# Kernel tuning notes

Hardware: AMD Instinct MI355X
Metric: run time of the kernel (lower is better)

The kernel has to match this reference:

```python
import jax, jax.numpy as jnp
import numpy as np
from jax import lax

B, NF, NOBJ, SZ = 16, 4, 32, 128
HALF = SZ // 2  # 64


def _build_grid(h, w):
    ys = jnp.linspace(0.0, 1.0, h)
    xs = jnp.linspace(0.0, 1.0, w)
    gy, gx = jnp.meshgrid(ys, xs, indexing='ij')
    g = jnp.stack([gy, gx], axis=-1)  # (H, W, 2)
    return jnp.concatenate([g, 1.0 - g], axis=-1)[None]  # (1, H, W, 4)


def setup_inputs() -> dict:
    key = jax.random.key(0)
    ks = jax.random.split(key, 8)
    images = jax.random.normal(ks[0], (B, 3 * NF, SZ, SZ), dtype=jnp.float32)
    rois = jax.random.randint(ks[1], (B, NOBJ, SZ, SZ), 0, 2).astype(jnp.bool_)
    conv1_w = jax.random.normal(ks[2], (64, 3 * NF, 3, 3), dtype=jnp.float32) * 0.05
    conv1_b = jnp.zeros((64,), dtype=jnp.float32)
    conv2_w = jax.random.normal(ks[3], (128, 64, 3, 3), dtype=jnp.float32) * 0.05
    conv2_b = jnp.zeros((128,), dtype=jnp.float32)
    dense_w = jax.random.normal(ks[4], (128, 4), dtype=jnp.float32) * 0.1
    dense_b = jnp.zeros((128,), dtype=jnp.float32)
    return dict(images=images, rois=rois, conv1_w=conv1_w, conv1_b=conv1_b,
                conv2_w=conv2_w, conv2_b=conv2_b, dense_w=dense_w, dense_b=dense_b)


def _conv(x, w, b):
    y = lax.conv_general_dilated(x, w, window_strides=(1, 1), padding='SAME',
                                 dimension_numbers=('NCHW', 'OIHW', 'NCHW'))
    return y + b[None, :, None, None]


def reference(images, rois, conv1_w, conv1_b, conv2_w, conv2_b, dense_w, dense_b):
    # conv stack
    x = jax.nn.relu(_conv(images, conv1_w, conv1_b))
    x = lax.reduce_window(x, -jnp.inf, lax.max, (1, 1, 2, 2), (1, 1, 2, 2), 'VALID')
    x = jax.nn.relu(_conv(x, conv2_w, conv2_b))  # (B, 128, 64, 64)
    # soft position embed
    grid = _build_grid(HALF, HALF)  # (1, 64, 64, 4)
    pe = grid @ dense_w.T + dense_b  # (1, 64, 64, 128)
    x = x + jnp.transpose(pe, (0, 3, 1, 2))  # (B, 128, 64, 64)
    # roi pool: nearest-downsample masks 128->64 (indices 0,2,4,...)
    r = rois[:, :, ::2, ::2].astype(x.dtype)  # (B, O, 64, 64)
    masked = x[:, None] * r[:, :, None]  # (B, O, 128, 64, 64)
    return jnp.max(masked, axis=(-2, -1))  # (B, O, 128)
```

## Files before the change

### kernel.cpp

```cpp
#include <hip/hip_runtime.h>


typedef __attribute__((ext_vector_type(8))) short short8;
typedef __attribute__((ext_vector_type(4))) float f32x4;
typedef __attribute__((ext_vector_type(4))) unsigned short us4;
typedef __attribute__((ext_vector_type(2))) unsigned short u16x2;
typedef unsigned short u16;
typedef unsigned int u32;

__device__ __forceinline__ u16 f2bf(float f) {
  u32 u = __builtin_bit_cast(u32, f);
  return (u16)((u + 0x7fffu + ((u >> 16) & 1u)) >> 16);
}

__device__ __forceinline__ u32 pkmaxu(u32 a, u32 b) {
  u16x2 x = __builtin_bit_cast(u16x2, a), y = __builtin_bit_cast(u16x2, b);
  return __builtin_bit_cast(u32, __builtin_elementwise_max(x, y));
}
__device__ __forceinline__ u32 map2(u32 v) {
  u32 flip = ((v & 0x80008000u) >> 15) * 0xFFFFu;
  return v ^ (flip | 0x80008000u);
}
__device__ __forceinline__ float unmap1(u32 m) {
  u32 b = m ^ ((m & 0x8000u) ? 0x8000u : 0xFFFFu);
  return __builtin_bit_cast(float, b << 16);
}
__device__ __forceinline__ float fand(float x, u32 m) {
  return __builtin_bit_cast(float, __builtin_bit_cast(u32, x) & m);
}

namespace {

__global__ __launch_bounds__(256) void kio(const float* __restrict__ img,
                                           u16* __restrict__ imgT,
                                           const unsigned* __restrict__ rois,
                                           unsigned* __restrict__ rmask) {
  __shared__ alignas(16) u16 ST[2048];
  const int bx = blockIdx.x;
  const int t = threadIdx.x;
  if (bx < 2048) {
    const int row = bx & 127, b = bx >> 7;
#pragma unroll
    for (int i = 0; i < 2; ++i) {
      const int e = i * 256 + t;
      ST[(e >> 2) * 16 + 12 + (e & 3)] = 0;
    }
#pragma unroll
    for (int i = 0; i < 6; ++i) {
      const int e = i * 256 + t;
      const int ci = e >> 7, col = e & 127;
      const float v = img[(((size_t)(b * 12 + ci)) << 14) + row * 128 + col];
      ST[col * 16 + ci] = f2bf(v);
    }
    __syncthreads();
    us4* dst = (us4*)(imgT + (((size_t)(b * 128 + row)) << 11));
#pragma unroll
    for (int i = 0; i < 2; ++i) {
      const int q = i * 256 + t;
      dst[q] = *(const us4*)&ST[q * 4];
    }
  } else {
    const int lane = t & 63;
    u32 ok = 1u;
#pragma unroll
    for (int i = 0; i < 4; ++i) {
      u32 v = rois[lane * 4 + i];
      ok &= ((v <= 1u) || (v == 0x3f800000u)) ? 1u : 0u;
    }
    const bool isWord = (__all((int)ok) != 0);
    const unsigned char* roisB = (const unsigned char*)rois;
    const int pi = (bx - 2048) * 256 + t;
    const int b = pi >> 11;
    const int pp = pi & 2047;
    const int h = pp >> 5;
    const int wp = pp & 31;
    const size_t base = (size_t)b * 32 * 16384 + (size_t)(2 * h) * 128 + 4 * wp;
    u32 m0 = 0, m1 = 0;
#pragma unroll
    for (int o = 0; o < 32; ++o) {
      const size_t idx = base + (size_t)o * 16384;
      if (isWord) {
        const uint4 q = *(const uint4*)&rois[idx];
        m0 |= (u32)(q.x != 0u) << o;
        m1 |= (u32)(q.z != 0u) << o;
      } else {
        const u32 q = *(const u32*)&roisB[idx];
        m0 |= (u32)((q & 0xffu) != 0u) << o;
        m1 |= (u32)((q & 0xff0000u) != 0u) << o;
      }
    }
    *(uint2*)&rmask[b * 4096 + h * 64 + wp * 2] = make_uint2(m0, m1);
  }
}

__global__ __launch_bounds__(256) void kprep(const float* __restrict__ w2,
                                             u16* __restrict__ Aw,
                                             const float* __restrict__ w1,
                                             u16* __restrict__ Aw1) {
  const int bx = blockIdx.x;
  if (bx < 288) {
    const int idx = bx * 256 + threadIdx.x;
    const int j = idx & 7;
    const int lane = (idx >> 3) & 63;
    const int t3 = idx >> 9;
    const int ks = t3 % 18, cot = t3 / 18;
    const int m = lane & 15, g = lane >> 4;
    const int co = cot * 16 + m;
    const int k = ks * 32 + g * 8 + j;
    const int rc = k >> 6, ci = k & 63;
    Aw[idx] = f2bf(w2[co * 576 + ci * 9 + rc]);
  } else {
    const int idx = (bx - 288) * 256 + threadIdx.x;
    const int j = idx & 7;
    const int lane = (idx >> 3) & 63;
    const int t3 = idx >> 9;
    const int ks = t3 % 5, cot = t3 / 5;
    const int m = lane & 15, g = lane >> 4;
    const int co = cot * 16 + m;
    const int k = ks * 32 + g * 8 + j;
    const int rc = k >> 4, cip = k & 15;
    const float v = (rc < 9 && cip < 12) ? w1[co * 108 + cip * 9 + rc] : 0.f;
    Aw1[idx] = f2bf(v);
  }
}

__global__ __launch_bounds__(256) void k1_mfma(const u16* __restrict__ imgT,
                                               const u16* __restrict__ Aw1,
                                               const float* __restrict__ b1,
                                               u16* __restrict__ pooledT) {
  __shared__ alignas(16) u16 SIMG[8192];
  __shared__ alignas(16) u16 PT[64 * 68];
  const int h2 = blockIdx.x, b = blockIdx.y;
  const int t = threadIdx.x, wv = t >> 6, l = t & 63;

#pragma unroll
  for (int i = 0; i < 4; ++i) {
    const int q = i * 256 + t;
    const int sr = q >> 8, off = q & 255;
    const int irow = 2 * h2 - 1 + sr;
    short8 v = {0, 0, 0, 0, 0, 0, 0, 0};
    if ((unsigned)irow < 128u)
      v = *(const short8*)(imgT + (((size_t)(b * 128 + irow)) << 11) + off * 8);
    *(short8*)((char*)SIMG + ((q * 16) ^ (((q >> 3) & 1) << 4))) = v;
  }
  __syncthreads();

  const int m16 = l & 15, g = l >> 4;
  const int colhalf = wv >> 1, cotbase = (wv & 1) * 2;
  const int cipb = (g & 1) * 16;
  f32x4 acc[2][8];
#pragma unroll
  for (int ct = 0; ct < 2; ++ct)
#pragma unroll
    for (int pt = 0; pt < 8; ++pt) acc[ct][pt] = (f32x4){0.f, 0.f, 0.f, 0.f};

  const u16* awb = Aw1 + (size_t)l * 8;
  const short8 z8 = {0, 0, 0, 0, 0, 0, 0, 0};

#pragma unroll
  for (int ks = 0; ks < 5; ++ks) {
    short8 a0 = *(const short8*)(awb + (cotbase * 5 + ks) * 512);
    short8 a1 = *(const short8*)(awb + ((cotbase + 1) * 5 + ks) * 512);
    const bool pz = (ks == 4) && (g >= 2);
    const int rc = pz ? 0 : (2 * ks + (g >> 1));
    const int rr = (rc * 11) >> 5;
    const int cc = rc - rr * 3;
    const int d = m16 - 1 + cc;
    const int sb = (d < 0) ? 1 : ((d >> 2) & 1);
    const int base = rr * 4096 + d * 32 + colhalf * 2048 + (cipb ^ (sb << 4));
    const bool killLo = (cc == 0) && (m16 == 0) && (colhalf == 0);
    const bool killHi = (cc == 2) && (m16 == 15) && (colhalf == 1);
#pragma unroll
    for (int pt = 0; pt < 8; ++pt) {
      const int r01 = pt >> 2, ct2 = pt & 3;
      short8 bv = *(const short8*)((const char*)SIMG + base + r01 * 4096 + ct2 * 512);
      bool kill = pz;
      if (ct2 == 0) kill = kill || killLo;
      if (ct2 == 3) kill = kill || killHi;
      if (kill) bv = z8;
      acc[0][pt] = __builtin_amdgcn_mfma_f32_16x16x32_bf16(a0, bv, acc[0][pt], 0, 0, 0);
      acc[1][pt] = __builtin_amdgcn_mfma_f32_16x16x32_bf16(a1, bv, acc[1][pt], 0, 0, 0);
    }
  }

#pragma unroll
  for (int ct = 0; ct < 2; ++ct) {
    const int cot = cotbase + ct;
#pragma unroll
    for (int r = 0; r < 4; ++r) {
      const int co = cot * 16 + g * 4 + r;
      const float bias = b1[co];
#pragma unroll
      for (int ct2 = 0; ct2 < 4; ++ct2) {
        float v0 = fmaxf(acc[ct][ct2][r] + bias, 0.f);
        float v1 = fmaxf(acc[ct][4 + ct2][r] + bias, 0.f);
        float vv = fmaxf(v0, v1);
        vv = fmaxf(vv, __shfl_xor(vv, 1, 64));
        if (!(m16 & 1)) {
          const int pw = colhalf * 32 + ct2 * 8 + (m16 >> 1);
          PT[pw * 68 + co] = f2bf(vv);
        }
      }
    }
  }
  __syncthreads();
  u16* dst = pooledT + (((size_t)(b * 64 + h2)) << 12);
#pragma unroll
  for (int i = 0; i < 4; ++i) {
    const int e = (i * 256 + t) * 4;
    const int pw = e >> 6, co = e & 63;
    *(us4*)(dst + e) = *(const us4*)&PT[pw * 68 + co];
  }
}

__global__ __launch_bounds__(256) void k2_mfma(const u16* __restrict__ pooledT,
                                               const u16* __restrict__ Aw,
                                               const float* __restrict__ b2,
                                               const float* __restrict__ dw,
                                               const float* __restrict__ db,
                                               u16* __restrict__ x2b) {
  __shared__ alignas(16) short8 SIN8[1536];
  char* SB = (char*)SIN8;
  const int h = blockIdx.x, b = blockIdx.y;
  const int t = threadIdx.x, wv = t >> 6, l = t & 63;

#pragma unroll
  for (int i = 0; i < 6; ++i) {
    const int chunk = i * 4 + wv;
    const int row = chunk >> 3;
    const int hin = h - 1 + row;
    short8 v = {0, 0, 0, 0, 0, 0, 0, 0};
    if ((unsigned)hin < 64u)
      v = *(const short8*)(pooledT + (((size_t)(b * 64 + hin)) << 12) +
                           ((chunk & 7) << 9) + l * 8);
    const int lin = chunk * 1024 + l * 16;
    *(short8*)(SB + (lin ^ (((lin >> 7) & 7) << 4))) = v;
  }
  __syncthreads();

  const int m16 = l & 15, g = l >> 4;
  const int kbyte = g * 16;
  f32x4 acc[2][4];
#pragma unroll
  for (int ct = 0; ct < 2; ++ct)
#pragma unroll
    for (int n = 0; n < 4; ++n) acc[ct][n] = (f32x4){0.f, 0.f, 0.f, 0.f};

  const u16* aw0 = Aw + (size_t)wv * 36 * 512 + l * 8;
  const short8 z8 = {0, 0, 0, 0, 0, 0, 0, 0};

#pragma unroll
  for (int ks = 0; ks < 18; ++ks) {
    const int rc = ks >> 1, r = rc / 3, c = rc % 3;
    const int koff = r * 8192 + (ks & 1) * 64 + kbyte;
    short8 a0 = *(const short8*)(aw0 + ks * 512);
    short8 a1 = *(const short8*)(aw0 + (18 + ks) * 512);
    const int d = m16 + c - 1;
    const int base = (koff + d * 128) ^ ((d & 7) << 4);
    const bool edgeLo = (c == 0) && (m16 == 0);
    const bool edgeHi = (c == 2) && (m16 == 15);
#pragma unroll
    for (int n = 0; n < 4; ++n) {
      short8 bv = *(const short8*)(SB + base + n * 2048);
      if (c == 0 && n == 0) { if (edgeLo) bv = z8; }
      if (c == 2 && n == 3) { if (edgeHi) bv = z8; }
      acc[0][n] = __builtin_amdgcn_mfma_f32_16x16x32_bf16(a0, bv, acc[0][n], 0, 0, 0);
      acc[1][n] = __builtin_amdgcn_mfma_f32_16x16x32_bf16(a1, bv, acc[1][n], 0, 0, 0);
    }
  }

  const float inv63 = 1.f / 63.f;
  const float gy = (float)h * inv63;
#pragma unroll
  for (int ct = 0; ct < 2; ++ct) {
    const int cot = wv * 2 + ct;
#pragma unroll
    for (int r = 0; r < 4; ++r) {
      const int co = cot * 16 + g * 4 + r;
      const float bias = b2[co];
      const float W0 = dw[co * 4 + 0], W1 = dw[co * 4 + 1];
      const float W2 = dw[co * 4 + 2], W3 = dw[co * 4 + 3];
      const float pe0 = gy * (W0 - W2) + W2 + W3 + db[co];
      const float s13 = W1 - W3;
      u16* orow = x2b + (((size_t)(b * 128 + co)) << 12) + h * 64;
#pragma unroll
      for (int n = 0; n < 4; ++n) {
        const int w = n * 16 + m16;
        orow[w] = f2bf(fmaxf(acc[ct][n][r] + bias, 0.f) + pe0 + (float)w * inv63 * s13);
      }
    }
  }
}

__global__ __launch_bounds__(256) void k3_roi(const u16* __restrict__ x2b,
                                              const unsigned* __restrict__ rmask,
                                              u32* __restrict__ partial) {
  __shared__ alignas(16) char LB[18688];
  u32* XSU = (u32*)LB;
  u32* MS = (u32*)(LB + 16640);
  const int cg = blockIdx.x, pq = blockIdx.y, b = blockIdx.z;
  const int t = threadIdx.x, wv = t >> 6, lane = t & 63;
  const int p0 = pq * 512;

#pragma unroll
  for (int i = 0; i < 4; ++i) {
    const int f4 = i * 256 + t;
    const int c = f4 >> 6, cidx = f4 & 63;
    uint4 v = *(const uint4*)&x2b[(((size_t)(b * 128 + cg * 16 + c)) << 12) + p0 + cidx * 8];
    v.x = map2(v.x); v.y = map2(v.y); v.z = map2(v.z); v.w = map2(v.w);
    *(uint4*)&XSU[c * 260 + cidx * 4] = v;
  }
  if (t < 128) *(uint4*)&MS[t * 4] = *(const uint4*)&rmask[b * 4096 + p0 + t * 4];
  __syncthreads();

  const int og = lane >> 3, cu = lane & 7;
  const u32* r0 = XSU + (2 * cu) * 260;
  const u32* r1 = XSU + (2 * cu + 1) * 260;
  const int ps = wv * 128;

  u32 a[4][2];
#pragma unroll
  for (int r = 0; r < 4; ++r) { a[r][0] = 0u; a[r][1] = 0u; }

  for (int pi = 0; pi < 32; ++pi) {
    const int p = ps + pi * 4;
    const uint4 mw = *(const uint4*)&MS[p];
    const uint2 xa = *(const uint2*)&r0[p >> 1];
    const uint2 xb = *(const uint2*)&r1[p >> 1];
#pragma unroll
    for (int r = 0; r < 4; ++r) {
      const int o = og * 4 + r;
      u32 t0 = (u32)((int)(mw.x << (31 - o)) >> 31);
      u32 t1 = (u32)((int)(mw.y << (31 - o)) >> 31);
      u32 pm = (t0 & 0xFFFFu) | (t1 & 0xFFFF0000u);
      a[r][0] = pkmaxu(a[r][0], (xa.x & pm) | (0x80008000u & ~pm));
      a[r][1] = pkmaxu(a[r][1], (xb.x & pm) | (0x80008000u & ~pm));
      t0 = (u32)((int)(mw.z << (31 - o)) >> 31);
      t1 = (u32)((int)(mw.w << (31 - o)) >> 31);
      pm = (t0 & 0xFFFFu) | (t1 & 0xFFFF0000u);
      a[r][0] = pkmaxu(a[r][0], (xa.y & pm) | (0x80008000u & ~pm));
      a[r][1] = pkmaxu(a[r][1], (xb.y & pm) | (0x80008000u & ~pm));
    }
  }

  __syncthreads();
  u32* RED = (u32*)LB;
#pragma unroll
  for (int r = 0; r < 4; ++r) {
    RED[(wv * 64 + lane) * 8 + r * 2 + 0] = a[r][0];
    RED[(wv * 64 + lane) * 8 + r * 2 + 1] = a[r][1];
  }
  __syncthreads();
  {
    const int o = t >> 3, clp = t & 7;
    const int sl = (o >> 2) * 8 + clp;
    const int s0 = (o & 3) * 2;
    u32 m0 = 0u, m1 = 0u;
#pragma unroll
    for (int w = 0; w < 4; ++w) {
      const uint2 q = *(const uint2*)&RED[(w * 64 + sl) * 8 + s0];
      m0 = pkmaxu(m0, q.x);
      m1 = pkmaxu(m1, q.y);
    }
    u32 f0l = m0 & 0xFFFFu, f0h = m0 >> 16;
    u32 f1l = m1 & 0xFFFFu, f1h = m1 >> 16;
    const u32 f0 = f0l > f0h ? f0l : f0h;
    const u32 f1 = f1l > f1h ? f1l : f1h;
    partial[(size_t)pq * 32768 + ((size_t)b * 32 + o) * 64 + cg * 8 + clp] =
        f0 | (f1 << 16);
  }
}

__global__ __launch_bounds__(256) void k4_merge(const u32* __restrict__ partial,
                                                float* __restrict__ out) {
  const int idx = blockIdx.x * 256 + threadIdx.x;
  u32 v = partial[idx];
#pragma unroll
  for (int q = 1; q < 8; ++q) v = pkmaxu(v, partial[q * 32768 + idx]);
  float2 o2;
  o2.x = unmap1(v & 0xFFFFu);
  o2.y = unmap1(v >> 16);
  *(float2*)&out[idx * 2] = o2;
}

}

extern "C" void kernel_launch(void* const* d_in, const int* in_sizes, int n_in,
                              void* d_out, int out_size, void* d_ws, size_t ws_size,
                              hipStream_t stream) {
  const float* images = (const float*)d_in[0];
  const unsigned* rois = (const unsigned*)d_in[1];
  const float* w1 = (const float*)d_in[2];
  const float* b1 = (const float*)d_in[3];
  const float* w2 = (const float*)d_in[4];
  const float* b2 = (const float*)d_in[5];
  const float* dw = (const float*)d_in[6];
  const float* db = (const float*)d_in[7];
  float* out = (float*)d_out;

  char* ws = (char*)d_ws;
  unsigned* rmask = (unsigned*)(ws);
  u16* pooledT = (u16*)(ws + 0x40000);
  u16* Aw2 = (u16*)(ws + 0x840000);
  u16* Aw1 = (u16*)(ws + 0x864000);
  u16* imgT = (u16*)(ws + 0x900000);
  u16* x2b = (u16*)(ws + 0x900000);
  u32* partial = (u32*)(ws + 0x40000);

  hipLaunchKernelGGL(kio, dim3(2176), dim3(256), 0, stream, images, imgT, rois, rmask);
  hipLaunchKernelGGL(kprep, dim3(328), dim3(256), 0, stream, w2, Aw2, w1, Aw1);
  hipLaunchKernelGGL(k1_mfma, dim3(64, 16), dim3(256), 0, stream, imgT, Aw1, b1, pooledT);
  hipLaunchKernelGGL(k2_mfma, dim3(64, 16), dim3(256), 0, stream, pooledT, Aw2, b2, dw, db, x2b);
  hipLaunchKernelGGL(k3_roi, dim3(8, 8, 16), dim3(256), 0, stream, x2b, rmask, partial);
  hipLaunchKernelGGL(k4_merge, dim3(128), dim3(256), 0, stream, partial, out);
}
```

Baseline: 72.64 us.

## Compute two output rows per conv2 block and merge prep kernels

The conv2 MFMA kernel now computes two output rows per block, loading four input rows into shared memory and reusing each A-weight fragment across twice as many MFMAs. This halves the weight loads per output and cuts the grid to 32x16 blocks. The separate weight-prep kernel is folded into the image/ROI preprocessing kernel to save one launch. In exchange, accumulator registers double and shared memory per block grows, which may lower occupancy; the smaller grid (512 blocks) may also underfill the GPU.

```diff
diff --git a/kernel.cpp b/kernel.cpp
--- a/kernel.cpp
+++ b/kernel.cpp
@@ -12,7 +12,6 @@
   u32 u = __builtin_bit_cast(u32, f);
   return (u16)((u + 0x7fffu + ((u >> 16) & 1u)) >> 16);
 }
-
 __device__ __forceinline__ u32 pkmaxu(u32 a, u32 b) {
   u16x2 x = __builtin_bit_cast(u16x2, a), y = __builtin_bit_cast(u16x2, b);
   return __builtin_bit_cast(u32, __builtin_elementwise_max(x, y));
@@ -25,16 +24,17 @@
   u32 b = m ^ ((m & 0x8000u) ? 0x8000u : 0xFFFFu);
   return __builtin_bit_cast(float, b << 16);
 }
-__device__ __forceinline__ float fand(float x, u32 m) {
-  return __builtin_bit_cast(float, __builtin_bit_cast(u32, x) & m);
-}
 
 namespace {
 
-__global__ __launch_bounds__(256) void kio(const float* __restrict__ img,
-                                           u16* __restrict__ imgT,
-                                           const unsigned* __restrict__ rois,
-                                           unsigned* __restrict__ rmask) {
+__global__ __launch_bounds__(256) void kiop(const float* __restrict__ img,
+                                            u16* __restrict__ imgT,
+                                            const unsigned* __restrict__ rois,
+                                            unsigned* __restrict__ rmask,
+                                            const float* __restrict__ w2,
+                                            u16* __restrict__ Aw2,
+                                            const float* __restrict__ w1,
+                                            u16* __restrict__ Aw1) {
   __shared__ alignas(16) u16 ST[2048];
   const int bx = blockIdx.x;
   const int t = threadIdx.x;
@@ -59,7 +59,7 @@
       const int q = i * 256 + t;
       dst[q] = *(const us4*)&ST[q * 4];
     }
-  } else {
+  } else if (bx < 2176) {
     const int lane = t & 63;
     u32 ok = 1u;
 #pragma unroll
@@ -90,16 +90,8 @@
       }
     }
     *(uint2*)&rmask[b * 4096 + h * 64 + wp * 2] = make_uint2(m0, m1);
-  }
-}
-
-__global__ __launch_bounds__(256) void kprep(const float* __restrict__ w2,
-                                             u16* __restrict__ Aw,
-                                             const float* __restrict__ w1,
-                                             u16* __restrict__ Aw1) {
-  const int bx = blockIdx.x;
-  if (bx < 288) {
-    const int idx = bx * 256 + threadIdx.x;
+  } else if (bx < 2464) {
+    const int idx = (bx - 2176) * 256 + t;
     const int j = idx & 7;
     const int lane = (idx >> 3) & 63;
     const int t3 = idx >> 9;
@@ -108,9 +100,9 @@
     const int co = cot * 16 + m;
     const int k = ks * 32 + g * 8 + j;
     const int rc = k >> 6, ci = k & 63;
-    Aw[idx] = f2bf(w2[co * 576 + ci * 9 + rc]);
+    Aw2[idx] = f2bf(w2[co * 576 + ci * 9 + rc]);
   } else {
-    const int idx = (bx - 288) * 256 + threadIdx.x;
+    const int idx = (bx - 2464) * 256 + t;
     const int j = idx & 7;
     const int lane = (idx >> 3) & 63;
     const int t3 = idx >> 9;
@@ -219,16 +211,15 @@
                                                const float* __restrict__ dw,
                                                const float* __restrict__ db,
                                                u16* __restrict__ x2b) {
-  __shared__ alignas(16) short8 SIN8[1536];
-  char* SB = (char*)SIN8;
-  const int h = blockIdx.x, b = blockIdx.y;
+  __shared__ alignas(16) char SB[32768];
+  const int hp = blockIdx.x, b = blockIdx.y;
   const int t = threadIdx.x, wv = t >> 6, l = t & 63;
 
 #pragma unroll
-  for (int i = 0; i < 6; ++i) {
+  for (int i = 0; i < 8; ++i) {
     const int chunk = i * 4 + wv;
     const int row = chunk >> 3;
-    const int hin = h - 1 + row;
+    const int hin = 2 * hp - 1 + row;
     short8 v = {0, 0, 0, 0, 0, 0, 0, 0};
     if ((unsigned)hin < 64u)
       v = *(const short8*)(pooledT + (((size_t)(b * 64 + hin)) << 12) +
@@ -240,11 +231,11 @@
 
   const int m16 = l & 15, g = l >> 4;
   const int kbyte = g * 16;
-  f32x4 acc[2][4];
+  f32x4 acc[2][8];
 #pragma unroll
   for (int ct = 0; ct < 2; ++ct)
 #pragma unroll
-    for (int n = 0; n < 4; ++n) acc[ct][n] = (f32x4){0.f, 0.f, 0.f, 0.f};
+    for (int n = 0; n < 8; ++n) acc[ct][n] = (f32x4){0.f, 0.f, 0.f, 0.f};
 
   const u16* aw0 = Aw + (size_t)wv * 36 * 512 + l * 8;
   const short8 z8 = {0, 0, 0, 0, 0, 0, 0, 0};
@@ -260,17 +251,17 @@
     const bool edgeLo = (c == 0) && (m16 == 0);
     const bool edgeHi = (c == 2) && (m16 == 15);
 #pragma unroll
-    for (int n = 0; n < 4; ++n) {
-      short8 bv = *(const short8*)(SB + base + n * 2048);
-      if (c == 0 && n == 0) { if (edgeLo) bv = z8; }
-      if (c == 2 && n == 3) { if (edgeHi) bv = z8; }
+    for (int n = 0; n < 8; ++n) {
+      const int orw = n >> 2, n4 = n & 3;
+      short8 bv = *(const short8*)(SB + base + orw * 8192 + n4 * 2048);
+      if (c == 0 && n4 == 0) { if (edgeLo) bv = z8; }
+      if (c == 2 && n4 == 3) { if (edgeHi) bv = z8; }
       acc[0][n] = __builtin_amdgcn_mfma_f32_16x16x32_bf16(a0, bv, acc[0][n], 0, 0, 0);
       acc[1][n] = __builtin_amdgcn_mfma_f32_16x16x32_bf16(a1, bv, acc[1][n], 0, 0, 0);
     }
   }
 
   const float inv63 = 1.f / 63.f;
-  const float gy = (float)h * inv63;
 #pragma unroll
   for (int ct = 0; ct < 2; ++ct) {
     const int cot = wv * 2 + ct;
@@ -280,13 +271,19 @@
       const float bias = b2[co];
       const float W0 = dw[co * 4 + 0], W1 = dw[co * 4 + 1];
       const float W2 = dw[co * 4 + 2], W3 = dw[co * 4 + 3];
-      const float pe0 = gy * (W0 - W2) + W2 + W3 + db[co];
-      const float s13 = W1 - W3;
-      u16* orow = x2b + (((size_t)(b * 128 + co)) << 12) + h * 64;
-#pragma unroll
-      for (int n = 0; n < 4; ++n) {
-        const int w = n * 16 + m16;
-        orow[w] = f2bf(fmaxf(acc[ct][n][r] + bias, 0.f) + pe0 + (float)w * inv63 * s13);
+      const float c23 = W2 + W3 + db[co];
+      const float s02 = W0 - W2, s13 = W1 - W3;
+#pragma unroll
+      for (int orw = 0; orw < 2; ++orw) {
+        const int h = 2 * hp + orw;
+        const float pe0 = (float)h * inv63 * s02 + c23;
+        u16* orow = x2b + (((size_t)(b * 128 + co)) << 12) + h * 64;
+#pragma unroll
+        for (int n4 = 0; n4 < 4; ++n4) {
+          const int w = n4 * 16 + m16;
+          orow[w] = f2bf(fmaxf(acc[ct][orw * 4 + n4][r] + bias, 0.f) + pe0 +
+                         (float)w * inv63 * s13);
+        }
       }
     }
   }
@@ -407,10 +404,10 @@
   u16* x2b = (u16*)(ws + 0x900000);
   u32* partial = (u32*)(ws + 0x40000);
 
-  hipLaunchKernelGGL(kio, dim3(2176), dim3(256), 0, stream, images, imgT, rois, rmask);
-  hipLaunchKernelGGL(kprep, dim3(328), dim3(256), 0, stream, w2, Aw2, w1, Aw1);
+  hipLaunchKernelGGL(kiop, dim3(2504), dim3(256), 0, stream,
+                     images, imgT, rois, rmask, w2, Aw2, w1, Aw1);
   hipLaunchKernelGGL(k1_mfma, dim3(64, 16), dim3(256), 0, stream, imgT, Aw1, b1, pooledT);
-  hipLaunchKernelGGL(k2_mfma, dim3(64, 16), dim3(256), 0, stream, pooledT, Aw2, b2, dw, db, x2b);
+  hipLaunchKernelGGL(k2_mfma, dim3(32, 16), dim3(256), 0, stream, pooledT, Aw2, b2, dw, db, x2b);
   hipLaunchKernelGGL(k3_roi, dim3(8, 8, 16), dim3(256), 0, stream, x2b, rmask, partial);
   hipLaunchKernelGGL(k4_merge, dim3(128), dim3(256), 0, stream, partial, out);
 }
```

Result: no change. 71.62 us (-1.4%).
